# Performance work log

Hardware: AMD Instinct MI355X
Metric: run time of the kernel (lower is better)

The kernel has to match this reference:

```python
import jax, jax.numpy as jnp
import numpy as np

B, N, C = 256, 25, 256          # batch, joints, in_features
H = 256                          # hidden_features (MLP hidden = H // 2 = 128)


def _build_chain_paths(n):
    """Flatten shortest paths of a chain skeleton (parent[i]=i-1) into
    (heads, ends, pair_ids): edge k of path i->j contributes
    src[:, ends[e]] - src[:, heads[e]] accumulated into pair i*n+j."""
    heads, ends, pair = [], [], []
    for i in range(n):
        for j in range(n):
            step = 1 if j >= i else -1
            cur = i
            while cur != j:
                heads.append(cur)
                ends.append(cur + step)
                pair.append(i * n + j)
                cur += step
    return (np.asarray(heads, np.int32), np.asarray(ends, np.int32),
            np.asarray(pair, np.int32))


def setup_inputs() -> dict:
    key = jax.random.key(0)
    k_src, k_w1, k_w2 = jax.random.split(key, 3)
    heads, ends, pair_ids = _build_chain_paths(N)  # E = 5200 for N=25
    src = jax.random.normal(k_src, (B, N, C), dtype=jnp.float32)
    # torch Linear weights: [out, in], no bias for both edgefeat linears
    W1 = jax.random.normal(k_w1, (H // 2, C), dtype=jnp.float32) / np.sqrt(C)
    W2 = jax.random.normal(k_w2, (1, H // 2), dtype=jnp.float32) / np.sqrt(H // 2)
    alpha = jnp.full((1,), 0.25, dtype=jnp.float32)  # PReLU init
    return {"src": src, "heads": jnp.asarray(heads), "ends": jnp.asarray(ends),
            "pair_ids": jnp.asarray(pair_ids), "W1": W1, "alpha": alpha, "W2": W2}


def reference(src, heads, ends, pair_ids, W1, alpha, W2):
    b, n, c = src.shape
    # gather-subtract along every path edge: [B, E, C]
    diff = src[:, ends, :] - src[:, heads, :]
    # accumulate per (i, j) pair: segment_sum over leading axis -> [N*N, B, C]
    acc = jax.ops.segment_sum(jnp.transpose(diff, (1, 0, 2)), pair_ids,
                              num_segments=n * n)
    edge_feat = jnp.transpose(acc.reshape(n, n, b, c), (2, 0, 1, 3))  # [B,N,N,C]
    h = jnp.einsum('bijc,hc->bijh', edge_feat, W1)   # [B,N,N,H//2]
    h = jnp.where(h >= 0, h, alpha * h)              # PReLU (single shared alpha)
    return jnp.einsum('bijh,oh->bijo', h, W2)        # [B,N,N,1]
```

## Files before the change

### kernel.cpp

```cpp
#include <hip/hip_runtime.h>

#define NJ   25
#define CIN  256
#define HH   128

typedef __attribute__((ext_vector_type(8))) short short8;
typedef __attribute__((ext_vector_type(4))) float f32x4;

__device__ __forceinline__ unsigned short f2bf(float f) {
    union { float f; unsigned u; } v; v.f = f;
    unsigned r = v.u + 0x7FFF + ((v.u >> 16) & 1);
    return (unsigned short)(r >> 16);
}
__device__ __forceinline__ unsigned pack2(float a, float b) {
    return (unsigned)f2bf(a) | ((unsigned)f2bf(b) << 16);
}

__global__ __launch_bounds__(256) void prep_frags(
    const float* __restrict__ src, const float* __restrict__ W1,
    unsigned short* __restrict__ srcfrag, unsigned short* __restrict__ w1frag,
    int nsrc)
{
    const int gid = blockIdx.x * 256 + threadIdx.x;
    const float* base;
    unsigned short* dst;
    if (gid < nsrc) {
        const int lane = gid & 63, kt = (gid >> 6) & 7, mt = (gid >> 9) & 1, b = gid >> 10;
        const int row = mt * 16 + (lane & 15);
        const int k0  = kt * 32 + (lane >> 4) * 8;
        dst = srcfrag + (size_t)gid * 8;
        if (row >= NJ) { *(uint4*)dst = make_uint4(0u, 0u, 0u, 0u); return; }
        base = src + ((size_t)b * NJ + row) * CIN + k0;
    } else {
        const int id = gid - nsrc;
        if (id >= 4096) return;
        const int lane = id & 63, kt = (id >> 6) & 7, nt = id >> 9;
        const int row = nt * 16 + (lane & 15);
        const int k0  = kt * 32 + (lane >> 4) * 8;
        dst = w1frag + (size_t)id * 8;
        base = W1 + (size_t)row * CIN + k0;
    }
    float4 x = *(const float4*)base;
    float4 y = *(const float4*)(base + 4);
    uint4 o;
    o.x = pack2(x.x, x.y); o.y = pack2(x.z, x.w);
    o.z = pack2(y.x, y.y); o.w = pack2(y.z, y.w);
    *(uint4*)dst = o;
}

__global__ __launch_bounds__(512) void fused_edge_mlp_v4(
    const unsigned short* __restrict__ srcfrag,
    const unsigned short* __restrict__ w1frag,
    const float* __restrict__ Aarr,
    const float* __restrict__ W2,
    float* __restrict__ out)
{
    __shared__ float u_s[NJ * 132];

    const int b    = blockIdx.x;
    const int t    = threadIdx.x;
    const int w    = t >> 6;
    const int lane = t & 63;
    const int ln15 = lane & 15;
    const int quad = lane >> 4;

    {
        const short8* w1p = (const short8*)w1frag + (w * 8) * 64 + lane;
        const short8* ap  = (const short8*)srcfrag + ((size_t)b * 16) * 64 + lane;

        short8 bfrag[8];
        #pragma unroll
        for (int kt = 0; kt < 8; ++kt) bfrag[kt] = w1p[kt * 64];

        f32x4 acc0 = {0.f, 0.f, 0.f, 0.f};
        f32x4 acc1 = {0.f, 0.f, 0.f, 0.f};
        #pragma unroll
        for (int kt = 0; kt < 8; ++kt) {
            short8 a0 = ap[kt * 64];
            short8 a1 = ap[(8 + kt) * 64];
            acc0 = __builtin_amdgcn_mfma_f32_16x16x32_bf16(a0, bfrag[kt], acc0, 0, 0, 0);
            acc1 = __builtin_amdgcn_mfma_f32_16x16x32_bf16(a1, bfrag[kt], acc1, 0, 0, 0);
        }

        const int hcol = w * 16 + ln15;
        #pragma unroll
        for (int r = 0; r < 4; ++r) {
            int m0 = quad * 4 + r;
            if (m0 < NJ) u_s[m0 * 132 + hcol] = acc0[r];
            int m1 = 16 + quad * 4 + r;
            if (m1 < NJ) u_s[m1 * 132 + hcol] = acc1[r];
        }
    }
    __syncthreads();

    const float alpha = Aarr[0];
    float* outb = out + (size_t)b * (NJ * NJ);

    if (t < 300) {
        int i = (int)((49.0f - sqrtf(2401.0f - 8.0f * (float)t)) * 0.5f);
        {
            int Si = (49 * i - i * i) >> 1;
            if (t < Si) { --i; }
            else { int Sn = (49 * (i + 1) - (i + 1) * (i + 1)) >> 1; if (t >= Sn) ++i; }
        }
        const int S = (49 * i - i * i) >> 1;
        const int j = t - S + i + 1;

        const float* uj = u_s + j * 132;
        const float* ui = u_s + i * 132;
        const float4* w2v = (const float4*)W2;

        float M = 0.f, sj = 0.f, si = 0.f;
        #pragma unroll 8
        for (int h4 = 0; h4 < 32; ++h4) {
            float4 a = *(const float4*)(uj + h4 * 4);
            float4 c = *(const float4*)(ui + h4 * 4);
            float4 ww = w2v[h4];
            M  = fmaf(ww.x, fmaxf(a.x, c.x), M); sj = fmaf(ww.x, a.x, sj); si = fmaf(ww.x, c.x, si);
            M  = fmaf(ww.y, fmaxf(a.y, c.y), M); sj = fmaf(ww.y, a.y, sj); si = fmaf(ww.y, c.y, si);
            M  = fmaf(ww.z, fmaxf(a.z, c.z), M); sj = fmaf(ww.z, a.z, sj); si = fmaf(ww.z, c.z, si);
            M  = fmaf(ww.w, fmaxf(a.w, c.w), M); sj = fmaf(ww.w, a.w, sj); si = fmaf(ww.w, c.w, si);
        }
        const float Mw = (1.f - alpha) * M;
        outb[i * NJ + j] = Mw + alpha * sj - si;
        outb[j * NJ + i] = Mw + alpha * si - sj;
    } else if (t < 325) {
        const int i = t - 300;
        outb[i * (NJ + 1)] = 0.f;
    }
}

extern "C" void kernel_launch(void* const* d_in, const int* in_sizes, int n_in,
                              void* d_out, int out_size, void* d_ws, size_t ws_size,
                              hipStream_t stream) {
    const float* src   = (const float*)d_in[0];
    const float* W1    = (const float*)d_in[4];
    const float* alpha = (const float*)d_in[5];
    const float* W2    = (const float*)d_in[6];
    float* out = (float*)d_out;

    const int B    = in_sizes[0] / (NJ * CIN);
    const int nsrc = B * 16 * 64;
    unsigned short* srcfrag = (unsigned short*)d_ws;
    unsigned short* w1frag  = srcfrag + (size_t)nsrc * 8;

    const int totalA = nsrc + 4096;
    prep_frags<<<(totalA + 255) / 256, 256, 0, stream>>>(src, W1, srcfrag, w1frag, nsrc);
    fused_edge_mlp_v4<<<B, 512, 0, stream>>>(srcfrag, w1frag, alpha, W2, out);
}
```

Baseline: 74.62 us.

## Switch to fp16 MFMA, fp16 pair epilogue with dot2, hoist per-row sums

Converts the src, W1 and W2 fragments to fp16 instead of bf16, uses the f16 MFMA, and stores the projected features in LDS as fp16. The pairwise epilogue now uses packed half max plus fdot2 for the max term. The per-joint W2 dot products (si, sj) are computed once per row by separate threads and shared through LDS after an extra barrier, instead of being recomputed for every pair. This cuts LDS traffic and ALU work in the epilogue, at the cost of reduced precision and fp16 range risk, plus one more synchronisation.

```diff
diff --git a/kernel.cpp b/kernel.cpp
--- a/kernel.cpp
+++ b/kernel.cpp
@@ -3,23 +3,27 @@
 #define NJ   25
 #define CIN  256
 #define HH   128
+#define US   136
 
-typedef __attribute__((ext_vector_type(8))) short short8;
+typedef _Float16 h2  __attribute__((ext_vector_type(2)));
+typedef _Float16 h8f __attribute__((ext_vector_type(8)));
 typedef __attribute__((ext_vector_type(4))) float f32x4;
 
-__device__ __forceinline__ unsigned short f2bf(float f) {
-    union { float f; unsigned u; } v; v.f = f;
-    unsigned r = v.u + 0x7FFF + ((v.u >> 16) & 1);
-    return (unsigned short)(r >> 16);
+__device__ __forceinline__ unsigned short f2h_bits(float f) {
+    union { _Float16 h; unsigned short u; } v; v.h = (_Float16)f; return v.u;
 }
-__device__ __forceinline__ unsigned pack2(float a, float b) {
-    return (unsigned)f2bf(a) | ((unsigned)f2bf(b) << 16);
+__device__ __forceinline__ unsigned pack2h(float a, float b) {
+    return (unsigned)f2h_bits(a) | ((unsigned)f2h_bits(b) << 16);
+}
+__device__ __forceinline__ h2 as_h2(unsigned u) {
+    union { unsigned u; h2 h; } v; v.u = u; return v.h;
 }
 
 __global__ __launch_bounds__(256) void prep_frags(
     const float* __restrict__ src, const float* __restrict__ W1,
+    const float* __restrict__ W2,
     unsigned short* __restrict__ srcfrag, unsigned short* __restrict__ w1frag,
-    int nsrc)
+    unsigned* __restrict__ w2pk, int nsrc)
 {
     const int gid = blockIdx.x * 256 + threadIdx.x;
     const float* base;
@@ -31,31 +35,35 @@
         dst = srcfrag + (size_t)gid * 8;
         if (row >= NJ) { *(uint4*)dst = make_uint4(0u, 0u, 0u, 0u); return; }
         base = src + ((size_t)b * NJ + row) * CIN + k0;
-    } else {
+    } else if (gid < nsrc + 4096) {
         const int id = gid - nsrc;
-        if (id >= 4096) return;
         const int lane = id & 63, kt = (id >> 6) & 7, nt = id >> 9;
         const int row = nt * 16 + (lane & 15);
         const int k0  = kt * 32 + (lane >> 4) * 8;
         dst = w1frag + (size_t)id * 8;
         base = W1 + (size_t)row * CIN + k0;
+    } else {
+        const int id = gid - nsrc - 4096;
+        if (id < HH / 2) w2pk[id] = pack2h(W2[2 * id], W2[2 * id + 1]);
+        return;
     }
     float4 x = *(const float4*)base;
     float4 y = *(const float4*)(base + 4);
     uint4 o;
-    o.x = pack2(x.x, x.y); o.y = pack2(x.z, x.w);
-    o.z = pack2(y.x, y.y); o.w = pack2(y.z, y.w);
+    o.x = pack2h(x.x, x.y); o.y = pack2h(x.z, x.w);
+    o.z = pack2h(y.x, y.y); o.w = pack2h(y.z, y.w);
     *(uint4*)dst = o;
 }
 
-__global__ __launch_bounds__(512) void fused_edge_mlp_v4(
+__global__ __launch_bounds__(512) void fused_edge_mlp_v6(
     const unsigned short* __restrict__ srcfrag,
     const unsigned short* __restrict__ w1frag,
+    const unsigned* __restrict__ w2pk,
     const float* __restrict__ Aarr,
-    const float* __restrict__ W2,
     float* __restrict__ out)
 {
-    __shared__ float u_s[NJ * 132];
+    __shared__ unsigned short u16[NJ * US];
+    __shared__ float s_s[NJ];
 
     const int b    = blockIdx.x;
     const int t    = threadIdx.x;
@@ -63,12 +71,13 @@
     const int lane = t & 63;
     const int ln15 = lane & 15;
     const int quad = lane >> 4;
+    const int hcol = w * 16 + ln15;
 
     {
-        const short8* w1p = (const short8*)w1frag + (w * 8) * 64 + lane;
-        const short8* ap  = (const short8*)srcfrag + ((size_t)b * 16) * 64 + lane;
+        const h8f* w1p = (const h8f*)w1frag + (w * 8) * 64 + lane;
+        const h8f* ap  = (const h8f*)srcfrag + ((size_t)b * 16) * 64 + lane;
 
-        short8 bfrag[8];
+        h8f bfrag[8];
         #pragma unroll
         for (int kt = 0; kt < 8; ++kt) bfrag[kt] = w1p[kt * 64];
 
@@ -76,57 +85,75 @@
         f32x4 acc1 = {0.f, 0.f, 0.f, 0.f};
         #pragma unroll
         for (int kt = 0; kt < 8; ++kt) {
-            short8 a0 = ap[kt * 64];
-            short8 a1 = ap[(8 + kt) * 64];
-            acc0 = __builtin_amdgcn_mfma_f32_16x16x32_bf16(a0, bfrag[kt], acc0, 0, 0, 0);
-            acc1 = __builtin_amdgcn_mfma_f32_16x16x32_bf16(a1, bfrag[kt], acc1, 0, 0, 0);
+            acc0 = __builtin_amdgcn_mfma_f32_16x16x32_f16(ap[kt * 64],       bfrag[kt], acc0, 0, 0, 0);
+            acc1 = __builtin_amdgcn_mfma_f32_16x16x32_f16(ap[(8 + kt) * 64], bfrag[kt], acc1, 0, 0, 0);
         }
 
-        const int hcol = w * 16 + ln15;
         #pragma unroll
         for (int r = 0; r < 4; ++r) {
             int m0 = quad * 4 + r;
-            if (m0 < NJ) u_s[m0 * 132 + hcol] = acc0[r];
+            if (m0 < NJ) u16[m0 * US + hcol] = f2h_bits(acc0[r]);
             int m1 = 16 + quad * 4 + r;
-            if (m1 < NJ) u_s[m1 * 132 + hcol] = acc1[r];
+            if (m1 < NJ) u16[m1 * US + hcol] = f2h_bits(acc1[r]);
         }
     }
     __syncthreads();
 
     const float alpha = Aarr[0];
     float* outb = out + (size_t)b * (NJ * NJ);
+    const uint4* w2v = (const uint4*)w2pk;
 
+    float M = 0.f;
+    int i = 0, j = 0;
     if (t < 300) {
-        int i = (int)((49.0f - sqrtf(2401.0f - 8.0f * (float)t)) * 0.5f);
+        i = (int)((49.0f - sqrtf(2401.0f - 8.0f * (float)t)) * 0.5f);
         {
             int Si = (49 * i - i * i) >> 1;
             if (t < Si) { --i; }
             else { int Sn = (49 * (i + 1) - (i + 1) * (i + 1)) >> 1; if (t >= Sn) ++i; }
         }
         const int S = (49 * i - i * i) >> 1;
-        const int j = t - S + i + 1;
+        j = t - S + i + 1;
 
-        const float* uj = u_s + j * 132;
-        const float* ui = u_s + i * 132;
-        const float4* w2v = (const float4*)W2;
+        const uint4* ujp = (const uint4*)(u16 + j * US);
+        const uint4* uip = (const uint4*)(u16 + i * US);
+        #pragma unroll
+        for (int h8 = 0; h8 < 16; ++h8) {
+            uint4 a = ujp[h8], c = uip[h8], ww = w2v[h8];
+            h2 mx;
+            mx = __builtin_elementwise_max(as_h2(a.x), as_h2(c.x));
+            M  = __builtin_amdgcn_fdot2(mx, as_h2(ww.x), M, false);
+            mx = __builtin_elementwise_max(as_h2(a.y), as_h2(c.y));
+            M  = __builtin_amdgcn_fdot2(mx, as_h2(ww.y), M, false);
+            mx = __builtin_elementwise_max(as_h2(a.z), as_h2(c.z));
+            M  = __builtin_amdgcn_fdot2(mx, as_h2(ww.z), M, false);
+            mx = __builtin_elementwise_max(as_h2(a.w), as_h2(c.w));
+            M  = __builtin_amdgcn_fdot2(mx, as_h2(ww.w), M, false);
+        }
+    } else if (t < 300 + NJ) {
+        const int r = t - 300;
+        const uint4* up = (const uint4*)(u16 + r * US);
+        float s = 0.f;
+        #pragma unroll
+        for (int h8 = 0; h8 < 16; ++h8) {
+            uint4 a = up[h8], ww = w2v[h8];
+            s = __builtin_amdgcn_fdot2(as_h2(a.x), as_h2(ww.x), s, false);
+            s = __builtin_amdgcn_fdot2(as_h2(a.y), as_h2(ww.y), s, false);
+            s = __builtin_amdgcn_fdot2(as_h2(a.z), as_h2(ww.z), s, false);
+            s = __builtin_amdgcn_fdot2(as_h2(a.w), as_h2(ww.w), s, false);
+        }
+        s_s[r] = s;
+    }
+    __syncthreads();
 
-        float M = 0.f, sj = 0.f, si = 0.f;
-        #pragma unroll 8
-        for (int h4 = 0; h4 < 32; ++h4) {
-            float4 a = *(const float4*)(uj + h4 * 4);
-            float4 c = *(const float4*)(ui + h4 * 4);
-            float4 ww = w2v[h4];
-            M  = fmaf(ww.x, fmaxf(a.x, c.x), M); sj = fmaf(ww.x, a.x, sj); si = fmaf(ww.x, c.x, si);
-            M  = fmaf(ww.y, fmaxf(a.y, c.y), M); sj = fmaf(ww.y, a.y, sj); si = fmaf(ww.y, c.y, si);
-            M  = fmaf(ww.z, fmaxf(a.z, c.z), M); sj = fmaf(ww.z, a.z, sj); si = fmaf(ww.z, c.z, si);
-            M  = fmaf(ww.w, fmaxf(a.w, c.w), M); sj = fmaf(ww.w, a.w, sj); si = fmaf(ww.w, c.w, si);
-        }
+    if (t < 300) {
+        const float sj = s_s[j], si = s_s[i];
         const float Mw = (1.f - alpha) * M;
         outb[i * NJ + j] = Mw + alpha * sj - si;
         outb[j * NJ + i] = Mw + alpha * si - sj;
-    } else if (t < 325) {
-        const int i = t - 300;
-        outb[i * (NJ + 1)] = 0.f;
+    } else if (t >= 325 && t < 350) {
+        const int r = t - 325;
+        outb[r * (NJ + 1)] = 0.f;
     }
 }
 
@@ -143,8 +170,9 @@
     const int nsrc = B * 16 * 64;
     unsigned short* srcfrag = (unsigned short*)d_ws;
     unsigned short* w1frag  = srcfrag + (size_t)nsrc * 8;
+    unsigned*       w2pk    = (unsigned*)(w1frag + 4096 * 8);
 
-    const int totalA = nsrc + 4096;
-    prep_frags<<<(totalA + 255) / 256, 256, 0, stream>>>(src, W1, srcfrag, w1frag, nsrc);
-    fused_edge_mlp_v4<<<B, 512, 0, stream>>>(srcfrag, w1frag, alpha, W2, out);
+    const int totalA = nsrc + 4096 + HH / 2;
+    prep_frags<<<(totalA + 255) / 256, 256, 0, stream>>>(src, W1, W2, srcfrag, w1frag, w2pk, nsrc);
+    fused_edge_mlp_v6<<<B, 512, 0, stream>>>(srcfrag, w1frag, w2pk, alpha, out);
 }
```

After: 73.76 us. Within noise of the previous version (-1.2%).
